# Kernel tuning notes

Measured on AMD Instinct MI355X. Metric: run time of the kernel, lower is better.

Reference implementation:

```python
import jax, jax.numpy as jnp
import numpy as np

B, S, D, H, E, K = 4, 2048, 1024, 2048, 8, 2
TEMP = 5.0
EPS = 1e-9


def setup_inputs() -> dict:
    key = jax.random.key(0)
    k_x, k_wg, k_w1, k_w2 = jax.random.split(key, 4)
    scale = 0.02
    return {
        "x": jax.random.normal(k_x, (B, S, D), dtype=jnp.float32),
        "Wg": jax.random.normal(k_wg, (D, E), dtype=jnp.float32) * scale,
        "bg": jnp.zeros((E,), dtype=jnp.float32),
        "W1": jax.random.normal(k_w1, (E, D, H), dtype=jnp.float32) * scale,
        "b1": jnp.zeros((E, H), dtype=jnp.float32),
        "W2": jax.random.normal(k_w2, (E, H, D), dtype=jnp.float32) * scale,
        "b2": jnp.zeros((E, D), dtype=jnp.float32),
    }


def reference(x, Wg, bg, W1, b1, W2, b2):
    # Gating: softmax over experts with temperature
    logits = jnp.einsum('bsd,de->bse', x, Wg) + bg  # [B,S,E]
    probs = jax.nn.softmax(logits / TEMP, axis=-1)
    # Top-k mask, renormalized (zeros for non-selected experts)
    vals, idx = jax.lax.top_k(probs, K)              # [B,S,K]
    onehot = jax.nn.one_hot(idx, E, dtype=x.dtype)   # [B,S,K,E]
    mask = jnp.einsum('bske,bsk->bse', onehot, vals) # scatter topk values
    gates = mask / (jnp.sum(mask, axis=-1, keepdims=True) + EPS)
    # Expert FFNs (dense over experts; gate weight is exactly 0 for unrouted)
    h = jax.nn.gelu(jnp.einsum('bsd,edh->besh', x, W1) + b1[None, :, None, :],
                    approximate=False)               # [B,E,S,H]
    out = jnp.einsum('besh,ehd->besd', h, W2) + b2[None, :, None, :]
    y = jnp.einsum('bse,besd->bsd', gates, out)      # weighted combine
    return y
```

## Files before the change

### kernel.cpp

```cpp
#include <hip/hip_runtime.h>
#include <stdint.h>

#define NTOK 8192
#define DIM  1024
#define HID  2048
#define NE   8
#define CAP  17408
#define TM 128
#define TN 128
#define TKK 64

typedef __bf16  bf16x8  __attribute__((ext_vector_type(8)));
typedef float   floatx4 __attribute__((ext_vector_type(4)));

__device__ __forceinline__ unsigned short f2bf(float f) {
  union { float f; unsigned u; } v; v.f = f;
  unsigned r = v.u + 0x7FFFu + ((v.u >> 16) & 1u);
  return (unsigned short)(r >> 16);
}

__device__ __forceinline__ void async_ld16(const unsigned short* g, unsigned short* l) {
  __builtin_amdgcn_global_load_lds(
      (const __attribute__((address_space(1))) unsigned int*)(const void*)g,
      (__attribute__((address_space(3))) unsigned int*)(void*)l, 16, 0, 0);
}

__device__ __forceinline__ float gelu_fast(float v) {
  float g = 0.79788456080286536f * (v + 0.044715f * v * v * v);
  float t = __builtin_amdgcn_exp2f(-2.8853900817779268f * g);
  return v * __builtin_amdgcn_rcpf(1.0f + t);
}

__device__ __forceinline__ uint2 pack4bf(float a, float b, float c, float d) {
  uint2 o;
  o.x = (unsigned)f2bf(a) | ((unsigned)f2bf(b) << 16);
  o.y = (unsigned)f2bf(c) | ((unsigned)f2bf(d) << 16);
  return o;
}

__global__ void transpose_cast_kernel(const float* __restrict__ src,
                                      unsigned short* __restrict__ dst,
                                      int R, int C) {
  __shared__ unsigned short T[64][65];
  int e = blockIdx.z;
  const float* S = src + (size_t)e * R * C;
  unsigned short* D2 = dst + (size_t)e * R * C;
  int c0 = blockIdx.x * 64;
  int r0 = blockIdx.y * 64;
  int col = threadIdx.x & 63;
  int rr  = threadIdx.x >> 6;
#pragma unroll
  for (int i = 0; i < 16; i++) {
    int r = rr + i * 4;
    T[col][r] = f2bf(S[(size_t)(r0 + r) * C + c0 + col]);
  }
  __syncthreads();
#pragma unroll
  for (int i = 0; i < 16; i++) {
    int r = rr + i * 4;
    D2[(size_t)(c0 + r) * R + r0 + col] = T[r][col];
  }
}

__global__ __launch_bounds__(256)
void gating_kernel(const float* __restrict__ x, const float* __restrict__ Wg,
                   const float* __restrict__ bg, int* __restrict__ tok_e,
                   float* __restrict__ tok_g, unsigned short* __restrict__ xb) {
  __shared__ float WgS[NE * DIM];
  int tid = threadIdx.x;
#pragma unroll
  for (int j = 0; j < NE * DIM / 256; j++) {
    int i = j * 256 + tid;
    WgS[(i & 7) * DIM + (i >> 3)] = Wg[i];
  }
  __syncthreads();
  int wave = tid >> 6;
  int lane = tid & 63;
#pragma unroll
  for (int ti = 0; ti < 2; ti++) {
    int t = blockIdx.x * 8 + wave * 2 + ti;
    const float* xr = x + (size_t)t * DIM;
    float p[NE];
#pragma unroll
    for (int e = 0; e < NE; e++) p[e] = 0.f;
#pragma unroll
    for (int it = 0; it < DIM / 256; it++) {
      int d = (it * 64 + lane) * 4;
      float4 xv = *(const float4*)&xr[d];
      *(uint2*)&xb[(size_t)t * DIM + d] = pack4bf(xv.x, xv.y, xv.z, xv.w);
#pragma unroll
      for (int e = 0; e < NE; e++) {
        float4 wv = *(const float4*)&WgS[e * DIM + d];
        p[e] += xv.x * wv.x + xv.y * wv.y + xv.z * wv.z + xv.w * wv.w;
      }
    }
#pragma unroll
    for (int e = 0; e < NE; e++) {
#pragma unroll
      for (int off = 32; off > 0; off >>= 1) p[e] += __shfl_xor(p[e], off);
    }
    if (lane == 0) {
      float s[NE];
      float m = -1e30f;
#pragma unroll
      for (int e = 0; e < NE; e++) { s[e] = (p[e] + bg[e]) * 0.2f; m = fmaxf(m, s[e]); }
      float sum = 0.f;
#pragma unroll
      for (int e = 0; e < NE; e++) { s[e] = expf(s[e] - m); sum += s[e]; }
      float inv = 1.0f / sum;
      int i0 = 0; float v0 = -1.f;
#pragma unroll
      for (int e = 0; e < NE; e++) { float pe = s[e] * inv; if (pe > v0) { v0 = pe; i0 = e; } }
      int i1 = -1; float v1 = -1.f;
#pragma unroll
      for (int e = 0; e < NE; e++) {
        if (e == i0) continue;
        float pe = s[e] * inv; if (pe > v1) { v1 = pe; i1 = e; }
      }
      float den = v0 + v1 + 1e-9f;
      tok_e[t * 2]     = i0; tok_g[t * 2]     = v0 / den;
      tok_e[t * 2 + 1] = i1; tok_g[t * 2 + 1] = v1 / den;
    }
  }
}

__global__ __launch_bounds__(256)
void count_kernel(const int* __restrict__ tok_e, int* __restrict__ cnt) {
  __shared__ int hist[NE];
  int tid = threadIdx.x;
  if (tid < NE) hist[tid] = 0;
  __syncthreads();
  int i0 = blockIdx.x * 512 + tid;
  atomicAdd(&hist[tok_e[i0]], 1);
  atomicAdd(&hist[tok_e[i0 + 256]], 1);
  __syncthreads();
  if (tid < NE) atomicAdd(&cnt[tid], hist[tid]);
}

__global__ void offsets_kernel(const int* __restrict__ cnt, int* __restrict__ seg) {
  if (threadIdx.x == 0 && blockIdx.x == 0) {
    int s = 0;
    for (int e = 0; e < NE; e++) { seg[e] = s; s += ((cnt[e] + TM - 1) / TM) * TM; }
    seg[NE] = s;
  }
}

__global__ __launch_bounds__(256)
void route_kernel(const int* __restrict__ tok_e, const float* __restrict__ tok_g,
                  const int* __restrict__ seg, int* __restrict__ cnt2,
                  int* __restrict__ token_row, float* __restrict__ gate_row,
                  int* __restrict__ tok_pos) {
  __shared__ int hist[NE];
  __shared__ int base[NE];
  int tid = threadIdx.x;
  if (tid < NE) hist[tid] = 0;
  __syncthreads();
  int t = blockIdx.x * 256 + tid;
  int e0 = tok_e[t * 2];
  int e1 = tok_e[t * 2 + 1];
  int r0 = atomicAdd(&hist[e0], 1);
  int r1 = atomicAdd(&hist[e1], 1);
  __syncthreads();
  if (tid < NE) base[tid] = atomicAdd(&cnt2[tid], hist[tid]);
  __syncthreads();
  int p0 = seg[e0] + base[e0] + r0;
  int p1 = seg[e1] + base[e1] + r1;
  token_row[p0] = t; gate_row[p0] = tok_g[t * 2];     tok_pos[t * 2]     = p0;
  token_row[p1] = t; gate_row[p1] = tok_g[t * 2 + 1]; tok_pos[t * 2 + 1] = p1;
}

__global__ __launch_bounds__(256, 3)
void gemm1_kernel(const unsigned short* __restrict__ xb, const unsigned short* __restrict__ w1t,
                  const float* __restrict__ b1, const int* __restrict__ token_row,
                  const int* __restrict__ seg, const unsigned short* __restrict__ zbuf,
                  unsigned short* __restrict__ hbuf) {
  __shared__ __align__(16) unsigned short As[TM * TKK];
  __shared__ __align__(16) unsigned short Bs[TN * TKK];
  int row0 = blockIdx.y * TM;
  int total = seg[NE];
  if (row0 >= total) return;
  int e = 0;
  while (row0 >= seg[e + 1]) e++;
  int n0 = blockIdx.x * TN;
  int tid = threadIdx.x;
  int lane = tid & 63;
  int w = tid >> 6;
  int wm = w >> 1;
  int wn = w & 1;
  int lrow = lane >> 3;
  int lk   = (lane & 7) * 8;

  floatx4 zero4 = {0.f, 0.f, 0.f, 0.f};
  floatx4 acc[4][4];
#pragma unroll
  for (int a = 0; a < 4; a++)
#pragma unroll
    for (int b = 0; b < 4; b++) acc[a][b] = zero4;

  const unsigned short* w1e = w1t + (size_t)e * DIM * HID;
  const unsigned short* srcA[4];
  const unsigned short* srcB[4];
#pragma unroll
  for (int i = 0; i < 4; i++) {
    int r = w * 32 + i * 8 + lrow;
    int t = token_row[row0 + r];
    srcA[i] = (t >= 0 ? xb + (size_t)t * DIM : zbuf) + lk;
  }
#pragma unroll
  for (int i = 0; i < 4; i++) {
    int r = w * 32 + i * 8 + lrow;
    srcB[i] = w1e + (size_t)(n0 + r) * DIM + lk;
  }

  int mr = lane & 15;
  int kq = (lane >> 4) * 8;

  for (int k0 = 0; k0 < DIM; k0 += TKK) {
#pragma unroll
    for (int i = 0; i < 4; i++)
      async_ld16(srcA[i] + k0, &As[(w * 32 + i * 8 + lrow) * TKK + lk]);
#pragma unroll
    for (int i = 0; i < 4; i++)
      async_ld16(srcB[i] + k0, &Bs[(w * 32 + i * 8 + lrow) * TKK + lk]);
    __syncthreads();
#pragma unroll
    for (int kk = 0; kk < TKK; kk += 32) {
      bf16x8 af[4], bfr[4];
#pragma unroll
      for (int im = 0; im < 4; im++)
        af[im] = *(const bf16x8*)&As[(wm * 64 + im * 16 + mr) * TKK + kk + kq];
#pragma unroll
      for (int in = 0; in < 4; in++)
        bfr[in] = *(const bf16x8*)&Bs[(wn * 64 + in * 16 + mr) * TKK + kk + kq];
#pragma unroll
      for (int im = 0; im < 4; im++)
#pragma unroll
        for (int in = 0; in < 4; in++)
          acc[im][in] = __builtin_amdgcn_mfma_f32_16x16x32_bf16(bfr[in], af[im], acc[im][in], 0, 0, 0);
    }
    __syncthreads();
  }
  int quad = lane >> 4;
  int c16 = lane & 15;
  const float* b1e = b1 + e * HID;
#pragma unroll
  for (int im = 0; im < 4; im++) {
    int r = row0 + wm * 64 + im * 16 + c16;
#pragma unroll
    for (int in = 0; in < 4; in++) {
      int c = n0 + wn * 64 + in * 16 + quad * 4;
      float4 bias = *(const float4*)&b1e[c];
      float v0 = gelu_fast(acc[im][in][0] + bias.x);
      float v1 = gelu_fast(acc[im][in][1] + bias.y);
      float v2 = gelu_fast(acc[im][in][2] + bias.z);
      float v3 = gelu_fast(acc[im][in][3] + bias.w);
      *(uint2*)&hbuf[(size_t)r * HID + c] = pack4bf(v0, v1, v2, v3);
    }
  }
}

__global__ __launch_bounds__(256, 3)
void gemm2_kernel(const unsigned short* __restrict__ hbuf, const unsigned short* __restrict__ w2t,
                  const float* __restrict__ b2, const float* __restrict__ gate_row,
                  const int* __restrict__ seg, unsigned short* __restrict__ obuf) {
  __shared__ __align__(16) unsigned short As[TM * TKK];
  __shared__ __align__(16) unsigned short Bs[TN * TKK];
  int row0 = blockIdx.y * TM;
  int total = seg[NE];
  if (row0 >= total) return;
  int e = 0;
  while (row0 >= seg[e + 1]) e++;
  int n0 = blockIdx.x * TN;
  int tid = threadIdx.x;
  int lane = tid & 63;
  int w = tid >> 6;
  int wm = w >> 1;
  int wn = w & 1;
  int lrow = lane >> 3;
  int lk   = (lane & 7) * 8;

  floatx4 zero4 = {0.f, 0.f, 0.f, 0.f};
  floatx4 acc[4][4];
#pragma unroll
  for (int a = 0; a < 4; a++)
#pragma unroll
    for (int b = 0; b < 4; b++) acc[a][b] = zero4;

  const unsigned short* w2e = w2t + (size_t)e * DIM * HID;
  const unsigned short* srcA[4];
  const unsigned short* srcB[4];
#pragma unroll
  for (int i = 0; i < 4; i++) {
    int r = w * 32 + i * 8 + lrow;
    srcA[i] = hbuf + (size_t)(row0 + r) * HID + lk;
  }
#pragma unroll
  for (int i = 0; i < 4; i++) {
    int r = w * 32 + i * 8 + lrow;
    srcB[i] = w2e + (size_t)(n0 + r) * HID + lk;
  }

  int mr = lane & 15;
  int kq = (lane >> 4) * 8;

  for (int k0 = 0; k0 < HID; k0 += TKK) {
#pragma unroll
    for (int i = 0; i < 4; i++)
      async_ld16(srcA[i] + k0, &As[(w * 32 + i * 8 + lrow) * TKK + lk]);
#pragma unroll
    for (int i = 0; i < 4; i++)
      async_ld16(srcB[i] + k0, &Bs[(w * 32 + i * 8 + lrow) * TKK + lk]);
    __syncthreads();
#pragma unroll
    for (int kk = 0; kk < TKK; kk += 32) {
      bf16x8 af[4], bfr[4];
#pragma unroll
      for (int im = 0; im < 4; im++)
        af[im] = *(const bf16x8*)&As[(wm * 64 + im * 16 + mr) * TKK + kk + kq];
#pragma unroll
      for (int in = 0; in < 4; in++)
        bfr[in] = *(const bf16x8*)&Bs[(wn * 64 + in * 16 + mr) * TKK + kk + kq];
#pragma unroll
      for (int im = 0; im < 4; im++)
#pragma unroll
        for (int in = 0; in < 4; in++)
          acc[im][in] = __builtin_amdgcn_mfma_f32_16x16x32_bf16(bfr[in], af[im], acc[im][in], 0, 0, 0);
    }
    __syncthreads();
  }
  int quad = lane >> 4;
  int c16 = lane & 15;
  const float* b2e = b2 + e * DIM;
#pragma unroll
  for (int im = 0; im < 4; im++) {
    int r = row0 + wm * 64 + im * 16 + c16;
    float gs = gate_row[r];
#pragma unroll
    for (int in = 0; in < 4; in++) {
      int c = n0 + wn * 64 + in * 16 + quad * 4;
      float4 bias = *(const float4*)&b2e[c];
      float v0 = gs * (acc[im][in][0] + bias.x);
      float v1 = gs * (acc[im][in][1] + bias.y);
      float v2 = gs * (acc[im][in][2] + bias.z);
      float v3 = gs * (acc[im][in][3] + bias.w);
      *(uint2*)&obuf[(size_t)r * DIM + c] = pack4bf(v0, v1, v2, v3);
    }
  }
}

__global__ void combine_kernel(const unsigned short* __restrict__ obuf,
                               const int* __restrict__ tok_pos,
                               float* __restrict__ y) {
  int idx = blockIdx.x * 256 + threadIdx.x;
  int t = idx >> 7;
  int c = (idx & 127) << 3;
  int p0 = tok_pos[t * 2];
  int p1 = tok_pos[t * 2 + 1];
  uint4 a = *(const uint4*)(obuf + (size_t)p0 * DIM + c);
  uint4 b = *(const uint4*)(obuf + (size_t)p1 * DIM + c);
  float out[8];
  unsigned au[4] = {a.x, a.y, a.z, a.w};
  unsigned bu[4] = {b.x, b.y, b.z, b.w};
#pragma unroll
  for (int i = 0; i < 4; i++) {
    union { unsigned u; float f; } lo0, hi0, lo1, hi1;
    lo0.u = au[i] << 16; hi0.u = au[i] & 0xFFFF0000u;
    lo1.u = bu[i] << 16; hi1.u = bu[i] & 0xFFFF0000u;
    out[i * 2]     = lo0.f + lo1.f;
    out[i * 2 + 1] = hi0.f + hi1.f;
  }
  float* yp = y + (size_t)t * DIM + c;
  *(float4*)yp       = *(float4*)&out[0];
  *(float4*)(yp + 4) = *(float4*)&out[4];
}

extern "C" void kernel_launch(void* const* d_in, const int* in_sizes, int n_in,
                              void* d_out, int out_size, void* d_ws, size_t ws_size,
                              hipStream_t stream) {
  const float* x  = (const float*)d_in[0];
  const float* Wg = (const float*)d_in[1];
  const float* bg = (const float*)d_in[2];
  const float* W1 = (const float*)d_in[3];
  const float* b1 = (const float*)d_in[4];
  const float* W2 = (const float*)d_in[5];
  const float* b2 = (const float*)d_in[6];
  float* y = (float*)d_out;
  char* ws = (char*)d_ws;

  constexpr size_t OFF_META = 0;
  constexpr size_t OFF_TOKE = 256;
  constexpr size_t OFF_TOKG = OFF_TOKE + (size_t)NTOK * 2 * 4;
  constexpr size_t OFF_TPOS = OFF_TOKG + (size_t)NTOK * 2 * 4;
  constexpr size_t OFF_TROW = OFF_TPOS + (size_t)NTOK * 2 * 4;
  constexpr size_t OFF_GROW = OFF_TROW + (size_t)CAP * 4;
  constexpr size_t OFF_ZB   = OFF_GROW + (size_t)CAP * 4;
  constexpr size_t OFF_XB   = OFF_ZB  + (size_t)DIM * 2;
  constexpr size_t OFF_W1T  = OFF_XB  + (size_t)NTOK * DIM * 2;
  constexpr size_t OFF_W2T  = OFF_W1T + (size_t)NE * DIM * HID * 2;
  constexpr size_t OFF_H    = OFF_W2T + (size_t)NE * DIM * HID * 2;
  constexpr size_t OFF_OBUF = OFF_XB;

  int* cnt        = (int*)(ws + OFF_META);
  int* cnt2       = (int*)(ws + OFF_META + 64);
  int* seg        = (int*)(ws + OFF_META + 128);
  int* tok_e      = (int*)(ws + OFF_TOKE);
  float* tok_g    = (float*)(ws + OFF_TOKG);
  int* tok_pos    = (int*)(ws + OFF_TPOS);
  int* token_row  = (int*)(ws + OFF_TROW);
  float* gate_row = (float*)(ws + OFF_GROW);
  unsigned short* zbuf = (unsigned short*)(ws + OFF_ZB);
  unsigned short* xb   = (unsigned short*)(ws + OFF_XB);
  unsigned short* w1t  = (unsigned short*)(ws + OFF_W1T);
  unsigned short* w2t  = (unsigned short*)(ws + OFF_W2T);
  unsigned short* hbuf = (unsigned short*)(ws + OFF_H);
  unsigned short* obuf = (unsigned short*)(ws + OFF_OBUF);

  hipMemsetAsync(ws, 0, 192, stream);
  hipMemsetAsync(token_row, 0xFF, (size_t)CAP * 4, stream);
  hipMemsetAsync(zbuf, 0, (size_t)DIM * 2, stream);

  transpose_cast_kernel<<<dim3(HID / 64, DIM / 64, NE), 256, 0, stream>>>(W1, w1t, DIM, HID);
  transpose_cast_kernel<<<dim3(DIM / 64, HID / 64, NE), 256, 0, stream>>>(W2, w2t, HID, DIM);
  gating_kernel<<<NTOK / 8, 256, 0, stream>>>(x, Wg, bg, tok_e, tok_g, xb);
  count_kernel<<<NTOK * 2 / 512, 256, 0, stream>>>(tok_e, cnt);
  offsets_kernel<<<1, 64, 0, stream>>>(cnt, seg);
  route_kernel<<<NTOK / 256, 256, 0, stream>>>(tok_e, tok_g, seg, cnt2, token_row, gate_row, tok_pos);
  gemm1_kernel<<<dim3(HID / TN, CAP / TM), 256, 0, stream>>>(xb, w1t, b1, token_row, seg, zbuf, hbuf);
  gemm2_kernel<<<dim3(DIM / TN, CAP / TM), 256, 0, stream>>>(hbuf, w2t, b2, gate_row, seg, obuf);
  combine_kernel<<<NTOK * DIM / 8 / 256, 256, 0, stream>>>(obuf, tok_pos, y);
}
```

Before: 438.0 us.

## Merge setup kernels, fold memsets in, and vectorize the weight transpose

Merges the two weight transpose/cast launches into one grid that also zeroes the metadata and zero-buffer, replacing the memset calls. The transpose now reads with float4 loads and writes 16-byte packed bf16 stores instead of scalar 2-byte accesses. The expert histogram moves into the gating kernel, and the segment-offset scan moves into the route kernel, which also fills padding rows with -1 and gate 0. The aim is fewer launches and memsets and better memory efficiency in the transpose. In exchange, every route block recomputes the offsets and writes the padding redundantly.

```diff
diff --git a/kernel.cpp b/kernel.cpp
--- a/kernel.cpp
+++ b/kernel.cpp
@@ -38,36 +38,66 @@
   return o;
 }
 
-__global__ void transpose_cast_kernel(const float* __restrict__ src,
-                                      unsigned short* __restrict__ dst,
-                                      int R, int C) {
+__global__ __launch_bounds__(256)
+void transpose_all_kernel(const float* __restrict__ W1, const float* __restrict__ W2,
+                          unsigned short* __restrict__ w1t, unsigned short* __restrict__ w2t,
+                          int* __restrict__ meta, unsigned short* __restrict__ zbuf) {
   __shared__ unsigned short T[64][65];
-  int e = blockIdx.z;
-  const float* S = src + (size_t)e * R * C;
-  unsigned short* D2 = dst + (size_t)e * R * C;
-  int c0 = blockIdx.x * 64;
-  int r0 = blockIdx.y * 64;
-  int col = threadIdx.x & 63;
-  int rr  = threadIdx.x >> 6;
-#pragma unroll
-  for (int i = 0; i < 16; i++) {
-    int r = rr + i * 4;
-    T[col][r] = f2bf(S[(size_t)(r0 + r) * C + c0 + col]);
-  }
-  __syncthreads();
-#pragma unroll
-  for (int i = 0; i < 16; i++) {
-    int r = rr + i * 4;
-    D2[(size_t)(c0 + r) * R + r0 + col] = T[r][col];
+  int z = blockIdx.z;
+  int tid = threadIdx.x;
+  if (z == 0 && blockIdx.x == 0 && blockIdx.y == 0) {
+    if (tid < 48) meta[tid] = 0;
+    uint2 zz = {0u, 0u};
+    *(uint2*)&zbuf[tid * 4] = zz;
+  }
+  const float* S;
+  unsigned short* D2;
+  int R, C, c0, r0;
+  if (z < 8) {
+    S = W1 + (size_t)z * DIM * HID;
+    D2 = w1t + (size_t)z * DIM * HID;
+    R = DIM; C = HID; c0 = blockIdx.x * 64; r0 = blockIdx.y * 64;
+  } else {
+    S = W2 + (size_t)(z - 8) * DIM * HID;
+    D2 = w2t + (size_t)(z - 8) * DIM * HID;
+    R = HID; C = DIM; c0 = blockIdx.y * 64; r0 = blockIdx.x * 64;
+  }
+  int lr = tid >> 4;
+  int lc = (tid & 15) * 4;
+#pragma unroll
+  for (int i = 0; i < 4; i++) {
+    int r = lr + i * 16;
+    float4 v = *(const float4*)&S[(size_t)(r0 + r) * C + c0 + lc];
+    T[lc + 0][r] = f2bf(v.x);
+    T[lc + 1][r] = f2bf(v.y);
+    T[lc + 2][r] = f2bf(v.z);
+    T[lc + 3][r] = f2bf(v.w);
+  }
+  __syncthreads();
+  int sc = tid >> 3;
+  int sr = (tid & 7) * 8;
+#pragma unroll
+  for (int i = 0; i < 2; i++) {
+    int c = sc + i * 32;
+    const unsigned short* p = &T[c][sr];
+    uint4 o;
+    o.x = (unsigned)p[0] | ((unsigned)p[1] << 16);
+    o.y = (unsigned)p[2] | ((unsigned)p[3] << 16);
+    o.z = (unsigned)p[4] | ((unsigned)p[5] << 16);
+    o.w = (unsigned)p[6] | ((unsigned)p[7] << 16);
+    *(uint4*)&D2[(size_t)(c0 + c) * R + r0 + sr] = o;
   }
 }
 
 __global__ __launch_bounds__(256)
 void gating_kernel(const float* __restrict__ x, const float* __restrict__ Wg,
                    const float* __restrict__ bg, int* __restrict__ tok_e,
-                   float* __restrict__ tok_g, unsigned short* __restrict__ xb) {
+                   float* __restrict__ tok_g, unsigned short* __restrict__ xb,
+                   int* __restrict__ cnt) {
   __shared__ float WgS[NE * DIM];
+  __shared__ int ghist[NE];
   int tid = threadIdx.x;
+  if (tid < NE) ghist[tid] = 0;
 #pragma unroll
   for (int j = 0; j < NE * DIM / 256; j++) {
     int i = j * 256 + tid;
@@ -120,40 +150,32 @@
       float den = v0 + v1 + 1e-9f;
       tok_e[t * 2]     = i0; tok_g[t * 2]     = v0 / den;
       tok_e[t * 2 + 1] = i1; tok_g[t * 2 + 1] = v1 / den;
-    }
-  }
-}
-
-__global__ __launch_bounds__(256)
-void count_kernel(const int* __restrict__ tok_e, int* __restrict__ cnt) {
-  __shared__ int hist[NE];
-  int tid = threadIdx.x;
-  if (tid < NE) hist[tid] = 0;
-  __syncthreads();
-  int i0 = blockIdx.x * 512 + tid;
-  atomicAdd(&hist[tok_e[i0]], 1);
-  atomicAdd(&hist[tok_e[i0 + 256]], 1);
-  __syncthreads();
-  if (tid < NE) atomicAdd(&cnt[tid], hist[tid]);
-}
-
-__global__ void offsets_kernel(const int* __restrict__ cnt, int* __restrict__ seg) {
-  if (threadIdx.x == 0 && blockIdx.x == 0) {
-    int s = 0;
-    for (int e = 0; e < NE; e++) { seg[e] = s; s += ((cnt[e] + TM - 1) / TM) * TM; }
-    seg[NE] = s;
-  }
+      atomicAdd(&ghist[i0], 1);
+      atomicAdd(&ghist[i1], 1);
+    }
+  }
+  __syncthreads();
+  if (tid < NE) atomicAdd(&cnt[tid], ghist[tid]);
 }
 
 __global__ __launch_bounds__(256)
 void route_kernel(const int* __restrict__ tok_e, const float* __restrict__ tok_g,
-                  const int* __restrict__ seg, int* __restrict__ cnt2,
+                  const int* __restrict__ cnt, int* __restrict__ cnt2,
+                  int* __restrict__ seg_out,
                   int* __restrict__ token_row, float* __restrict__ gate_row,
                   int* __restrict__ tok_pos) {
   __shared__ int hist[NE];
   __shared__ int base[NE];
+  __shared__ int segs[NE + 1];
+  __shared__ int cnts[NE];
   int tid = threadIdx.x;
-  if (tid < NE) hist[tid] = 0;
+  if (tid < NE) { hist[tid] = 0; cnts[tid] = cnt[tid]; }
+  __syncthreads();
+  if (tid == 0) {
+    int s = 0;
+    for (int e = 0; e < NE; e++) { segs[e] = s; s += ((cnts[e] + TM - 1) / TM) * TM; }
+    segs[NE] = s;
+  }
   __syncthreads();
   int t = blockIdx.x * 256 + tid;
   int e0 = tok_e[t * 2];
@@ -163,10 +185,17 @@
   __syncthreads();
   if (tid < NE) base[tid] = atomicAdd(&cnt2[tid], hist[tid]);
   __syncthreads();
-  int p0 = seg[e0] + base[e0] + r0;
-  int p1 = seg[e1] + base[e1] + r1;
+  int p0 = segs[e0] + base[e0] + r0;
+  int p1 = segs[e1] + base[e1] + r1;
   token_row[p0] = t; gate_row[p0] = tok_g[t * 2];     tok_pos[t * 2]     = p0;
   token_row[p1] = t; gate_row[p1] = tok_g[t * 2 + 1]; tok_pos[t * 2 + 1] = p1;
+  if (tid <= NE) seg_out[tid] = segs[tid];
+#pragma unroll
+  for (int e = 0; e < NE; e++)
+    for (int i = segs[e] + cnts[e] + tid; i < segs[e + 1]; i += 256) {
+      token_row[i] = -1;
+      gate_row[i] = 0.f;
+    }
 }
 
 __global__ __launch_bounds__(256, 3)
@@ -415,16 +444,9 @@
   unsigned short* hbuf = (unsigned short*)(ws + OFF_H);
   unsigned short* obuf = (unsigned short*)(ws + OFF_OBUF);
 
-  hipMemsetAsync(ws, 0, 192, stream);
-  hipMemsetAsync(token_row, 0xFF, (size_t)CAP * 4, stream);
-  hipMemsetAsync(zbuf, 0, (size_t)DIM * 2, stream);
-
-  transpose_cast_kernel<<<dim3(HID / 64, DIM / 64, NE), 256, 0, stream>>>(W1, w1t, DIM, HID);
-  transpose_cast_kernel<<<dim3(DIM / 64, HID / 64, NE), 256, 0, stream>>>(W2, w2t, HID, DIM);
-  gating_kernel<<<NTOK / 8, 256, 0, stream>>>(x, Wg, bg, tok_e, tok_g, xb);
-  count_kernel<<<NTOK * 2 / 512, 256, 0, stream>>>(tok_e, cnt);
-  offsets_kernel<<<1, 64, 0, stream>>>(cnt, seg);
-  route_kernel<<<NTOK / 256, 256, 0, stream>>>(tok_e, tok_g, seg, cnt2, token_row, gate_row, tok_pos);
+  transpose_all_kernel<<<dim3(32, 16, 16), 256, 0, stream>>>(W1, W2, w1t, w2t, (int*)(ws + OFF_META), zbuf);
+  gating_kernel<<<NTOK / 8, 256, 0, stream>>>(x, Wg, bg, tok_e, tok_g, xb, cnt);
+  route_kernel<<<NTOK / 256, 256, 0, stream>>>(tok_e, tok_g, cnt, cnt2, seg, token_row, gate_row, tok_pos);
   gemm1_kernel<<<dim3(HID / TN, CAP / TM), 256, 0, stream>>>(xb, w1t, b1, token_row, seg, zbuf, hbuf);
   gemm2_kernel<<<dim3(DIM / TN, CAP / TM), 256, 0, stream>>>(hbuf, w2t, b2, gate_row, seg, obuf);
   combine_kernel<<<NTOK * DIM / 8 / 256, 256, 0, stream>>>(obuf, tok_pos, y);
```

Result: no change. 437.4 us (-0.1%).
